# Performance work log

Measured on AMD Instinct MI355X. Metric: run time of the kernel, lower is better.

Reference implementation:

```python
import jax, jax.numpy as jnp
import numpy as np

N_NODES = 50000
N_EDGES = 800000
H = 128       # num_hidden
NUM_INV = 32  # num_inv


def _glorot(key, shape):
    fan_in, fan_out = shape[0], shape[1]
    lim = np.sqrt(6.0 / (fan_in + fan_out)).astype(np.float32)
    return jax.random.uniform(key, shape, jnp.float32, -lim, lim)


def setup_inputs() -> dict:
    key = jax.random.key(0)
    ks = jax.random.split(key, 12)
    x = jax.random.normal(ks[0], (N_NODES, H), jnp.float32)
    adj = jax.random.randint(ks[1], (2, N_EDGES), 0, N_NODES, dtype=jnp.int64)
    inv = jax.random.normal(ks[2], (N_EDGES, NUM_INV), jnp.float32)
    # MessageLayer: message_mlp = Linear(2H+inv -> H), SiLU, Linear(H -> H), SiLU
    Wm1 = _glorot(ks[3], (2 * H + NUM_INV, H)); bm1 = jnp.zeros((H,), jnp.float32)
    Wm2 = _glorot(ks[4], (H, H));               bm2 = jnp.zeros((H,), jnp.float32)
    # edge_inf_mlp = Linear(H -> 1), Sigmoid
    We = _glorot(ks[5], (H, 1));                be = jnp.zeros((1,), jnp.float32)
    # UpdateLayer (num_mes=1): update_mlp = Linear(2H -> H), SiLU, Linear(H -> H)
    Wu1 = _glorot(ks[6], (2 * H, H));           bu1 = jnp.zeros((H,), jnp.float32)
    Wu2 = _glorot(ks[7], (H, H));               bu2 = jnp.zeros((H,), jnp.float32)
    return {"x": x, "adj": adj, "inv": inv,
            "Wm1": Wm1, "bm1": bm1, "Wm2": Wm2, "bm2": bm2,
            "We": We, "be": be,
            "Wu1": Wu1, "bu1": bu1, "Wu2": Wu2, "bu2": bu2}


def reference(x, adj, inv, Wm1, bm1, Wm2, bm2, We, be, Wu1, bu1, Wu2, bu2):
    send, rec = adj[0], adj[1]
    # MessageLayer: gather endpoints, concat with invariants, 2-layer SiLU MLP
    state = jnp.concatenate([x[send], x[rec], inv], axis=1)      # [E, 2H+inv]
    h = jax.nn.silu(state @ Wm1 + bm1)                           # [E, H]
    msg = jax.nn.silu(h @ Wm2 + bm2)                             # [E, H]
    gate = jax.nn.sigmoid(msg @ We + be)                         # [E, 1]
    aggr = jax.ops.segment_sum(msg * gate, rec, num_segments=x.shape[0])  # [N, H]
    # UpdateLayer: concat [x, aggregated message], Linear-SiLU-Linear
    upd_in = jnp.concatenate([x, aggr], axis=1)                  # [N, 2H]
    x_up = jax.nn.silu(upd_in @ Wu1 + bu1) @ Wu2 + bu2           # [N, H]
    # Residual add
    return x + x_up
```

## Files before the change

kernel.cpp:

```cpp
#include <hip/hip_runtime.h>
#include <math.h>

#define NNODES 50000
#define NEDGES 800000
#define HDIM 128
#define NINV 32
#define K1 288
#define NTILES_E 25000
#define NTILES_N 1563

#define W1STRIDE 296
#define U1STRIDE 264
#define HSTRIDE 132

typedef float floatx4 __attribute__((ext_vector_type(4)));
typedef short short8  __attribute__((ext_vector_type(8)));

union V4S8 { uint4 u; short8 s; int2 d[2]; };

__device__ __forceinline__ float silu_f(float z) { return z / (1.0f + __expf(-z)); }

__device__ __forceinline__ unsigned short f2bf_rne(float f) {
    unsigned u = __float_as_uint(f);
    u += 0x7fffu + ((u >> 16) & 1u);
    return (unsigned short)(u >> 16);
}

__device__ __forceinline__ unsigned pk_bf(float hi, float lo) {
    return __builtin_amdgcn_perm(__float_as_uint(hi), __float_as_uint(lo), 0x07060302);
}

__device__ __forceinline__ short8 cvt8(float4 f0, float4 f1) {
    V4S8 v;
    v.u.x = pk_bf(f0.y, f0.x);
    v.u.y = pk_bf(f0.w, f0.z);
    v.u.z = pk_bf(f1.y, f1.x);
    v.u.w = pk_bf(f1.w, f1.z);
    return v.s;
}

__device__ __forceinline__ int adj_at(const void* adj, int is64, long long pos) {
    if (is64) return (int)((const long long*)adj)[pos];
    return ((const int*)adj)[pos];
}

__global__ __launch_bounds__(256) void detect_idx64(const int* __restrict__ adj32,
                                                    int* __restrict__ flag) {
    __shared__ int any_nz;
    if (threadIdx.x == 0) any_nz = 0;
    __syncthreads();
    int v = adj32[threadIdx.x * 2 + 1];
    if (v != 0) atomicOr(&any_nz, 1);
    __syncthreads();
    if (threadIdx.x == 0) *flag = (any_nz == 0) ? 1 : 0;
}

__global__ __launch_bounds__(256) void prep_weights(
    const float* __restrict__ Wm1, const float* __restrict__ Wm2,
    const float* __restrict__ Wu1, const float* __restrict__ Wu2,
    unsigned short* __restrict__ Wm1t, unsigned short* __restrict__ Wm2t,
    unsigned short* __restrict__ Wu1t, unsigned short* __restrict__ Wu2t)
{
    int i = blockIdx.x * 256 + threadIdx.x;
    if (i < 128 * K1) {
        int n = i / K1, k = i % K1;
        Wm1t[i] = f2bf_rne(Wm1[k * HDIM + n]);
    } else if ((i -= 128 * K1) < 128 * HDIM) {
        int n = i / HDIM, k = i % HDIM;
        Wm2t[i] = f2bf_rne(Wm2[k * HDIM + n]);
    } else if ((i -= 128 * HDIM) < 128 * 256) {
        int n = i / 256, k = i % 256;
        Wu1t[i] = f2bf_rne(Wu1[k * HDIM + n]);
    } else if ((i -= 128 * 256) < 128 * HDIM) {
        int n = i / HDIM, k = i % HDIM;
        Wu2t[i] = f2bf_rne(Wu2[k * HDIM + n]);
    }
}

__global__ __launch_bounds__(512, 2) void edge_kernel(
    const float* __restrict__ x, const void* __restrict__ adj,
    const int* __restrict__ flagp, const float* __restrict__ inv,
    const unsigned short* __restrict__ Wm1t, const float* __restrict__ bm1,
    const unsigned short* __restrict__ Wm2t, const float* __restrict__ bm2,
    const float* __restrict__ We, const float* __restrict__ be,
    float* __restrict__ aggr)
{
    __shared__ unsigned short s_w1[128 * W1STRIDE];
    __shared__ unsigned short s_h[8 * 32 * HSTRIDE];

    const int t    = threadIdx.x;
    const int is64 = *flagp;
    const int l    = t & 63;
    const int wid  = t >> 6;
    const int l15  = l & 15;
    const int quad = l >> 4;

    for (int idx = t; idx < 128 * 36; idx += 512) {
        int n = idx / 36, c = idx % 36;
        *(uint4*)&s_w1[n * W1STRIDE + c * 8] = *(const uint4*)(Wm1t + n * K1 + c * 8);
    }

    short8 w2f[4][8];
    #pragma unroll
    for (int ks = 0; ks < 4; ++ks)
        #pragma unroll
        for (int nt = 0; nt < 8; ++nt)
            w2f[ks][nt] = *(const short8*)(Wm2t + (nt * 16 + l15) * HDIM + ks * 32 + quad * 8);

    __syncthreads();

    unsigned short* hbuf = s_h + wid * (32 * HSTRIDE);
    const int gwave  = blockIdx.x * 8 + wid;
    const int nwaves = gridDim.x * 8;

    for (int tile = gwave; tile < NTILES_E; tile += nwaves) {
        const int e0 = tile * 32;
        int se[2], re[2];
        unsigned offS[2], offR[2], offI[2];
        #pragma unroll
        for (int m = 0; m < 2; ++m) {
            se[m] = adj_at(adj, is64, e0 + m * 16 + l15);
            re[m] = adj_at(adj, is64, (long long)NEDGES + e0 + m * 16 + l15);
            offS[m] = (unsigned)se[m] * HDIM;
            offR[m] = (unsigned)re[m] * HDIM;
            offI[m] = (unsigned)(e0 + m * 16 + l15) * NINV;
        }

        auto aptr = [&](int s, int m) -> const float* {
            if (s < 4)  return x   + offS[m] + s * 32 + quad * 8;
            if (s < 8)  return x   + offR[m] + (s - 4) * 32 + quad * 8;
            return             inv + offI[m] + quad * 8;
        };

        float4 F0[2][2], F1[2][2];
        #pragma unroll
        for (int m = 0; m < 2; ++m) {
            const float* p = aptr(0, m); F0[m][0] = ((const float4*)p)[0]; F0[m][1] = ((const float4*)p)[1];
            const float* q = aptr(1, m); F1[m][0] = ((const float4*)q)[0]; F1[m][1] = ((const float4*)q)[1];
        }

        floatx4 acc[2][8];
        #pragma unroll
        for (int nt = 0; nt < 8; ++nt) {
            float bv = bm1[nt * 16 + l15];
            acc[0][nt] = (floatx4){bv, bv, bv, bv};
            acc[1][nt] = acc[0][nt];
        }

        #pragma unroll
        for (int s = 0; s < 9; ++s) {
            short8 a[2];
            #pragma unroll
            for (int m = 0; m < 2; ++m) {
                float4 f0 = (s & 1) ? F1[m][0] : F0[m][0];
                float4 f1 = (s & 1) ? F1[m][1] : F0[m][1];
                a[m] = cvt8(f0, f1);
                if (s + 2 <= 8) {
                    const float* p = aptr(s + 2, m);
                    if (s & 1) { F1[m][0] = ((const float4*)p)[0]; F1[m][1] = ((const float4*)p)[1]; }
                    else       { F0[m][0] = ((const float4*)p)[0]; F0[m][1] = ((const float4*)p)[1]; }
                }
            }
            const unsigned short* wbase = s_w1 + l15 * W1STRIDE + s * 32 + quad * 8;
            #pragma unroll
            for (int nt = 0; nt < 8; ++nt) {
                short8 b = *(const short8*)(wbase + nt * 16 * W1STRIDE);
                acc[0][nt] = __builtin_amdgcn_mfma_f32_16x16x32_bf16(a[0], b, acc[0][nt], 0, 0, 0);
                acc[1][nt] = __builtin_amdgcn_mfma_f32_16x16x32_bf16(a[1], b, acc[1][nt], 0, 0, 0);
            }
        }

        #pragma unroll
        for (int m = 0; m < 2; ++m)
            #pragma unroll
            for (int nt = 0; nt < 8; ++nt)
                #pragma unroll
                for (int r = 0; r < 4; ++r) {
                    float hv = silu_f(acc[m][nt][r]);
                    hbuf[(m * 16 + quad * 4 + r) * HSTRIDE + nt * 16 + l15] =
                        (unsigned short)(__float_as_uint(hv) >> 16);
                }

        #pragma unroll
        for (int nt = 0; nt < 8; ++nt) {
            float bv = bm2[nt * 16 + l15];
            acc[0][nt] = (floatx4){bv, bv, bv, bv};
            acc[1][nt] = acc[0][nt];
        }

        #pragma unroll
        for (int ks = 0; ks < 4; ++ks) {
            short8 a2[2];
            #pragma unroll
            for (int m = 0; m < 2; ++m) {
                int base = (m * 16 + l15) * HSTRIDE + ks * 32 + quad * 8;
                V4S8 v;
                v.d[0] = *(const int2*)(hbuf + base);
                v.d[1] = *(const int2*)(hbuf + base + 4);
                a2[m] = v.s;
            }
            #pragma unroll
            for (int nt = 0; nt < 8; ++nt) {
                acc[0][nt] = __builtin_amdgcn_mfma_f32_16x16x32_bf16(a2[0], w2f[ks][nt], acc[0][nt], 0, 0, 0);
                acc[1][nt] = __builtin_amdgcn_mfma_f32_16x16x32_bf16(a2[1], w2f[ks][nt], acc[1][nt], 0, 0, 0);
            }
        }

        float be0 = be[0];
        #pragma unroll
        for (int m = 0; m < 2; ++m) {
            #pragma unroll
            for (int nt = 0; nt < 8; ++nt)
                #pragma unroll
                for (int r = 0; r < 4; ++r)
                    acc[m][nt][r] = silu_f(acc[m][nt][r]);

            #pragma unroll
            for (int r = 0; r < 4; ++r) {
                float part = 0.f;
                #pragma unroll
                for (int nt = 0; nt < 8; ++nt)
                    part = fmaf(acc[m][nt][r], We[nt * 16 + l15], part);
                part += __shfl_xor(part, 1);
                part += __shfl_xor(part, 2);
                part += __shfl_xor(part, 4);
                part += __shfl_xor(part, 8);
                float g = 1.0f / (1.0f + __expf(-(part + be0)));
                int rr = __shfl(re[m], quad * 4 + r, 16);
                float* dst = aggr + (long long)rr * HDIM + l15;
                #pragma unroll
                for (int nt = 0; nt < 8; ++nt)
                    atomicAdd(dst + nt * 16, acc[m][nt][r] * g);
            }
        }
    }
}

__global__ __launch_bounds__(256) void node_kernel(
    const float* __restrict__ x, const float* __restrict__ aggr,
    const unsigned short* __restrict__ Wu1t, const float* __restrict__ bu1,
    const unsigned short* __restrict__ Wu2t, const float* __restrict__ bu2,
    float* __restrict__ out)
{
    __shared__ unsigned short s_u1[128 * U1STRIDE];
    __shared__ unsigned short s_h[4 * 32 * HSTRIDE];

    const int t    = threadIdx.x;
    const int l    = t & 63;
    const int wid  = t >> 6;
    const int l15  = l & 15;
    const int quad = l >> 4;

    for (int idx = t; idx < 128 * 32; idx += 256) {
        int n = idx / 32, c = idx % 32;
        *(uint4*)&s_u1[n * U1STRIDE + c * 8] = *(const uint4*)(Wu1t + n * 256 + c * 8);
    }

    short8 w2f[4][8];
    #pragma unroll
    for (int ks = 0; ks < 4; ++ks)
        #pragma unroll
        for (int nt = 0; nt < 8; ++nt)
            w2f[ks][nt] = *(const short8*)(Wu2t + (nt * 16 + l15) * HDIM + ks * 32 + quad * 8);

    __syncthreads();

    unsigned short* hbuf = s_h + wid * (32 * HSTRIDE);
    const int tile = blockIdx.x * 4 + wid;
    if (tile >= NTILES_N) return;
    const int n0 = tile * 32;

    unsigned offX[2];
    #pragma unroll
    for (int m = 0; m < 2; ++m) {
        int row = n0 + m * 16 + l15;
        if (row >= NNODES) row = NNODES - 1;
        offX[m] = (unsigned)row * HDIM;
    }

    floatx4 acc[2][8];
    #pragma unroll
    for (int nt = 0; nt < 8; ++nt) {
        float bv = bu1[nt * 16 + l15];
        acc[0][nt] = (floatx4){bv, bv, bv, bv};
        acc[1][nt] = acc[0][nt];
    }

    #pragma unroll
    for (int s = 0; s < 8; ++s) {
        short8 a[2];
        #pragma unroll
        for (int m = 0; m < 2; ++m) {
            const float* p = (s < 4) ? (x + offX[m] + s * 32 + quad * 8)
                                     : (aggr + offX[m] + (s - 4) * 32 + quad * 8);
            float4 f0 = ((const float4*)p)[0];
            float4 f1 = ((const float4*)p)[1];
            a[m] = cvt8(f0, f1);
        }
        const unsigned short* wbase = s_u1 + l15 * U1STRIDE + s * 32 + quad * 8;
        #pragma unroll
        for (int nt = 0; nt < 8; ++nt) {
            short8 b = *(const short8*)(wbase + nt * 16 * U1STRIDE);
            acc[0][nt] = __builtin_amdgcn_mfma_f32_16x16x32_bf16(a[0], b, acc[0][nt], 0, 0, 0);
            acc[1][nt] = __builtin_amdgcn_mfma_f32_16x16x32_bf16(a[1], b, acc[1][nt], 0, 0, 0);
        }
    }

    #pragma unroll
    for (int m = 0; m < 2; ++m)
        #pragma unroll
        for (int nt = 0; nt < 8; ++nt)
            #pragma unroll
            for (int r = 0; r < 4; ++r) {
                float hv = silu_f(acc[m][nt][r]);
                hbuf[(m * 16 + quad * 4 + r) * HSTRIDE + nt * 16 + l15] =
                    (unsigned short)(__float_as_uint(hv) >> 16);
            }

    #pragma unroll
    for (int nt = 0; nt < 8; ++nt) {
        float bv = bu2[nt * 16 + l15];
        acc[0][nt] = (floatx4){bv, bv, bv, bv};
        acc[1][nt] = acc[0][nt];
    }

    #pragma unroll
    for (int ks = 0; ks < 4; ++ks) {
        short8 a2[2];
        #pragma unroll
        for (int m = 0; m < 2; ++m) {
            int base = (m * 16 + l15) * HSTRIDE + ks * 32 + quad * 8;
            V4S8 v;
            v.d[0] = *(const int2*)(hbuf + base);
            v.d[1] = *(const int2*)(hbuf + base + 4);
            a2[m] = v.s;
        }
        #pragma unroll
        for (int nt = 0; nt < 8; ++nt) {
            acc[0][nt] = __builtin_amdgcn_mfma_f32_16x16x32_bf16(a2[0], w2f[ks][nt], acc[0][nt], 0, 0, 0);
            acc[1][nt] = __builtin_amdgcn_mfma_f32_16x16x32_bf16(a2[1], w2f[ks][nt], acc[1][nt], 0, 0, 0);
        }
    }

    #pragma unroll
    for (int m = 0; m < 2; ++m)
        #pragma unroll
        for (int r = 0; r < 4; ++r) {
            int row = n0 + m * 16 + quad * 4 + r;
            if (row < NNODES) {
                #pragma unroll
                for (int nt = 0; nt < 8; ++nt) {
                    int col = nt * 16 + l15;
                    out[(long long)row * HDIM + col] = x[(long long)row * HDIM + col] + acc[m][nt][r];
                }
            }
        }
}

extern "C" void kernel_launch(void* const* d_in, const int* in_sizes, int n_in,
                              void* d_out, int out_size, void* d_ws, size_t ws_size,
                              hipStream_t stream)
{
    const float* x   = (const float*)d_in[0];
    const void*  adj = d_in[1];
    const float* inv = (const float*)d_in[2];
    const float* Wm1 = (const float*)d_in[3];
    const float* bm1 = (const float*)d_in[4];
    const float* Wm2 = (const float*)d_in[5];
    const float* bm2 = (const float*)d_in[6];
    const float* We  = (const float*)d_in[7];
    const float* be  = (const float*)d_in[8];
    const float* Wu1 = (const float*)d_in[9];
    const float* bu1 = (const float*)d_in[10];
    const float* Wu2 = (const float*)d_in[11];
    const float* bu2 = (const float*)d_in[12];
    float* out = (float*)d_out;

    char* ws = (char*)d_ws;
    float* aggr = (float*)ws;
    size_t off = (size_t)NNODES * HDIM * 4;
    int* flag = (int*)(ws + off);            off += 16;
    unsigned short* Wm1t = (unsigned short*)(ws + off);  off += 128 * K1 * 2;
    unsigned short* Wm2t = (unsigned short*)(ws + off);  off += 128 * HDIM * 2;
    unsigned short* Wu1t = (unsigned short*)(ws + off);  off += 128 * 256 * 2;
    unsigned short* Wu2t = (unsigned short*)(ws + off);

    hipMemsetAsync(aggr, 0, (size_t)NNODES * HDIM * sizeof(float), stream);
    detect_idx64<<<1, 256, 0, stream>>>((const int*)adj, flag);
    prep_weights<<<400, 256, 0, stream>>>(Wm1, Wm2, Wu1, Wu2, Wm1t, Wm2t, Wu1t, Wu2t);
    edge_kernel<<<256, 512, 0, stream>>>(x, adj, flag, inv,
                                         Wm1t, bm1, Wm2t, bm2, We, be, aggr);
    node_kernel<<<(NTILES_N + 3) / 4, 256, 0, stream>>>(x, aggr,
                                                        Wu1t, bu1, Wu2t, bu2, out);
}
```

Baseline: 681.5 us.

## Sort edges by receiver and segment-reduce messages before atomic adds

Adds a counting sort of edges by receiver node (histogram, single-block scan, scatter) that produces sorted send/receive indices and a permutation used to gather the invariant features. In the edge kernel, each wave stages its gated messages in shared memory and does a run-length reduction over consecutive equal receivers. It then issues one atomic per run per column instead of one per edge. This targets the roughly one hundred million float atomics into the aggregation buffer. The cost is three extra preprocessing kernels, including a serial single-block scan, a randomised gather of inv rows, and extra shared-memory traffic. The gate weights are also hoisted into registers.

New measurement: 716.3 us. 5.1% more time.

```diff
diff --git a/kernel.cpp b/kernel.cpp
--- a/kernel.cpp
+++ b/kernel.cpp
@@ -12,6 +12,7 @@
 #define W1STRIDE 296
 #define U1STRIDE 264
 #define HSTRIDE 132
+#define FSTRIDE 66
 
 typedef float floatx4 __attribute__((ext_vector_type(4)));
 typedef short short8  __attribute__((ext_vector_type(8)));
@@ -77,9 +78,62 @@
     }
 }
 
+__global__ __launch_bounds__(256) void hist_kernel(const void* __restrict__ adj,
+                                                   const int* __restrict__ flagp,
+                                                   int* __restrict__ hist)
+{
+    int e = blockIdx.x * 256 + threadIdx.x;
+    if (e < NEDGES) {
+        int r = adj_at(adj, *flagp, (long long)NEDGES + e);
+        atomicAdd(&hist[r], 1);
+    }
+}
+
+__global__ __launch_bounds__(1024) void scan_kernel(const int* __restrict__ hist,
+                                                    int* __restrict__ cursor)
+{
+    __shared__ int sums[1024];
+    const int t = threadIdx.x;
+    const int CH = 49;
+    int lo = t * CH; if (lo > NNODES) lo = NNODES;
+    int hi = lo + CH; if (hi > NNODES) hi = NNODES;
+    int s = 0;
+    for (int i = lo; i < hi; ++i) s += hist[i];
+    sums[t] = s;
+    __syncthreads();
+    for (int d = 1; d < 1024; d <<= 1) {
+        int v = (t >= d) ? sums[t - d] : 0;
+        __syncthreads();
+        sums[t] += v;
+        __syncthreads();
+    }
+    int base = (t == 0) ? 0 : sums[t - 1];
+    for (int i = lo; i < hi; ++i) { cursor[i] = base; base += hist[i]; }
+}
+
+__global__ __launch_bounds__(256) void scatter_kernel(const void* __restrict__ adj,
+                                                      const int* __restrict__ flagp,
+                                                      int* __restrict__ cursor,
+                                                      int* __restrict__ sSend,
+                                                      int* __restrict__ sRec,
+                                                      int* __restrict__ perm)
+{
+    int e = blockIdx.x * 256 + threadIdx.x;
+    if (e < NEDGES) {
+        int is64 = *flagp;
+        int s = adj_at(adj, is64, e);
+        int r = adj_at(adj, is64, (long long)NEDGES + e);
+        int pos = atomicAdd(&cursor[r], 1);
+        sSend[pos] = s;
+        sRec[pos]  = r;
+        perm[pos]  = e;
+    }
+}
+
 __global__ __launch_bounds__(512, 2) void edge_kernel(
-    const float* __restrict__ x, const void* __restrict__ adj,
-    const int* __restrict__ flagp, const float* __restrict__ inv,
+    const float* __restrict__ x, const float* __restrict__ inv,
+    const int* __restrict__ sSend, const int* __restrict__ sRec,
+    const int* __restrict__ perm,
     const unsigned short* __restrict__ Wm1t, const float* __restrict__ bm1,
     const unsigned short* __restrict__ Wm2t, const float* __restrict__ bm2,
     const float* __restrict__ We, const float* __restrict__ be,
@@ -87,9 +141,9 @@
 {
     __shared__ unsigned short s_w1[128 * W1STRIDE];
     __shared__ unsigned short s_h[8 * 32 * HSTRIDE];
+    __shared__ int s_recb[8 * 32];
 
     const int t    = threadIdx.x;
-    const int is64 = *flagp;
     const int l    = t & 63;
     const int wid  = t >> 6;
     const int l15  = l & 15;
@@ -107,23 +161,30 @@
         for (int nt = 0; nt < 8; ++nt)
             w2f[ks][nt] = *(const short8*)(Wm2t + (nt * 16 + l15) * HDIM + ks * 32 + quad * 8);
 
+    float wev[8];
+    #pragma unroll
+    for (int nt = 0; nt < 8; ++nt) wev[nt] = We[nt * 16 + l15];
+    const float be0 = be[0];
+
     __syncthreads();
 
     unsigned short* hbuf = s_h + wid * (32 * HSTRIDE);
+    int* srec = s_recb + wid * 32;
     const int gwave  = blockIdx.x * 8 + wid;
     const int nwaves = gridDim.x * 8;
 
     for (int tile = gwave; tile < NTILES_E; tile += nwaves) {
         const int e0 = tile * 32;
-        int se[2], re[2];
+        int re[2];
         unsigned offS[2], offR[2], offI[2];
         #pragma unroll
         for (int m = 0; m < 2; ++m) {
-            se[m] = adj_at(adj, is64, e0 + m * 16 + l15);
-            re[m] = adj_at(adj, is64, (long long)NEDGES + e0 + m * 16 + l15);
-            offS[m] = (unsigned)se[m] * HDIM;
+            int idx = e0 + m * 16 + l15;
+            int se  = sSend[idx];
+            re[m]   = sRec[idx];
+            offS[m] = (unsigned)se * HDIM;
             offR[m] = (unsigned)re[m] * HDIM;
-            offI[m] = (unsigned)(e0 + m * 16 + l15) * NINV;
+            offI[m] = (unsigned)perm[idx] * NINV;
         }
 
         auto aptr = [&](int s, int m) -> const float* {
@@ -206,32 +267,59 @@
             }
         }
 
-        float be0 = be[0];
-        #pragma unroll
-        for (int m = 0; m < 2; ++m) {
+        #pragma unroll
+        for (int m = 0; m < 2; ++m)
             #pragma unroll
             for (int nt = 0; nt < 8; ++nt)
                 #pragma unroll
                 for (int r = 0; r < 4; ++r)
                     acc[m][nt][r] = silu_f(acc[m][nt][r]);
 
+        float g[2][4];
+        #pragma unroll
+        for (int m = 0; m < 2; ++m)
             #pragma unroll
             for (int r = 0; r < 4; ++r) {
                 float part = 0.f;
                 #pragma unroll
                 for (int nt = 0; nt < 8; ++nt)
-                    part = fmaf(acc[m][nt][r], We[nt * 16 + l15], part);
+                    part = fmaf(acc[m][nt][r], wev[nt], part);
                 part += __shfl_xor(part, 1);
                 part += __shfl_xor(part, 2);
                 part += __shfl_xor(part, 4);
                 part += __shfl_xor(part, 8);
-                float g = 1.0f / (1.0f + __expf(-(part + be0)));
-                int rr = __shfl(re[m], quad * 4 + r, 16);
-                float* dst = aggr + (long long)rr * HDIM + l15;
+                g[m][r] = 1.0f / (1.0f + __expf(-(part + be0)));
+            }
+
+        if (quad == 0) { srec[l15] = re[0]; srec[16 + l15] = re[1]; }
+
+        float* fred = (float*)hbuf;
+        #pragma unroll
+        for (int half = 0; half < 2; ++half) {
+            #pragma unroll
+            for (int m = 0; m < 2; ++m)
                 #pragma unroll
-                for (int nt = 0; nt < 8; ++nt)
-                    atomicAdd(dst + nt * 16, acc[m][nt][r] * g);
-            }
+                for (int nt2 = 0; nt2 < 4; ++nt2)
+                    #pragma unroll
+                    for (int r = 0; r < 4; ++r)
+                        fred[(m * 16 + quad * 4 + r) * FSTRIDE + nt2 * 16 + l15] =
+                            acc[m][half * 4 + nt2][r] * g[m][r];
+
+            float* dstbase = aggr + half * 64 + l;
+            float sum = 0.f;
+            int prev = srec[0];
+            #pragma unroll
+            for (int row = 0; row < 32; ++row) {
+                float v = fred[row * FSTRIDE + l];
+                int rc = srec[row];
+                if (rc != prev) {
+                    atomicAdd(dstbase + (unsigned)prev * HDIM, sum);
+                    sum = 0.f;
+                    prev = rc;
+                }
+                sum += v;
+            }
+            atomicAdd(dstbase + (unsigned)prev * HDIM, sum);
         }
     }
 }
@@ -383,12 +471,22 @@
     unsigned short* Wm1t = (unsigned short*)(ws + off);  off += 128 * K1 * 2;
     unsigned short* Wm2t = (unsigned short*)(ws + off);  off += 128 * HDIM * 2;
     unsigned short* Wu1t = (unsigned short*)(ws + off);  off += 128 * 256 * 2;
-    unsigned short* Wu2t = (unsigned short*)(ws + off);
+    unsigned short* Wu2t = (unsigned short*)(ws + off);  off += 128 * HDIM * 2;
+    int* hist   = (int*)(ws + off);          off += (size_t)NNODES * 4;
+    int* cursor = (int*)(ws + off);          off += (size_t)NNODES * 4;
+    int* sSend  = (int*)(ws + off);          off += (size_t)NEDGES * 4;
+    int* sRec   = (int*)(ws + off);          off += (size_t)NEDGES * 4;
+    int* perm   = (int*)(ws + off);          off += (size_t)NEDGES * 4;
 
     hipMemsetAsync(aggr, 0, (size_t)NNODES * HDIM * sizeof(float), stream);
+    hipMemsetAsync(hist, 0, (size_t)NNODES * sizeof(int), stream);
     detect_idx64<<<1, 256, 0, stream>>>((const int*)adj, flag);
     prep_weights<<<400, 256, 0, stream>>>(Wm1, Wm2, Wu1, Wu2, Wm1t, Wm2t, Wu1t, Wu2t);
-    edge_kernel<<<256, 512, 0, stream>>>(x, adj, flag, inv,
+    hist_kernel<<<(NEDGES + 255) / 256, 256, 0, stream>>>(adj, flag, hist);
+    scan_kernel<<<1, 1024, 0, stream>>>(hist, cursor);
+    scatter_kernel<<<(NEDGES + 255) / 256, 256, 0, stream>>>(adj, flag, cursor,
+                                                             sSend, sRec, perm);
+    edge_kernel<<<256, 512, 0, stream>>>(x, inv, sSend, sRec, perm,
                                          Wm1t, bm1, Wm2t, bm2, We, be, aggr);
     node_kernel<<<(NTILES_N + 3) / 4, 256, 0, stream>>>(x, aggr,
                                                         Wu1t, bu1, Wu2t, bu2, out);
```
